# Kernel optimization log

Hardware: AMD Instinct MI355X
Metric: run time of the kernel (lower is better)

## Reference

```python
import jax, jax.numpy as jnp
import numpy as np


def setup_inputs() -> dict:
    key = jax.random.key(0)
    k1, k2 = jax.random.split(key)
    B, S, D, O = 4, 4096, 2048, 2048
    inputs = jax.random.normal(k1, (B, S, D), dtype=jnp.float32)
    # truncated-normal-like init with stddev 1/sqrt(fan_in)
    w = jax.random.normal(k2, (D, O), dtype=jnp.float32) * (1.0 / np.sqrt(D))
    b = jnp.zeros((O,), dtype=jnp.float32)
    return {"inputs": inputs, "w": w, "b": b}


def reference(inputs, w, b):
    # logsumexp-semiring linear layer (basis=None path):
    #   out = log(exp(inputs - max_in) @ exp(w - max_w)) + max_in + max_w + b
    max_inputs = jnp.max(inputs)          # global scalar max for stabilization
    max_w = jnp.max(w)
    exp_inputs = jnp.exp(inputs - max_inputs)   # [B, S, D]
    exp_w = jnp.exp(w - max_w)                  # [D, O]
    out = jnp.log(jnp.dot(exp_inputs, exp_w))   # [B, S, O]
    out = out + (max_inputs + max_w)
    out = out + b                               # broadcast bias over [B, S, O]
    return out
```

## Files before the change

### kernel.cpp

```cpp
#include <hip/hip_runtime.h>

typedef int   i32x4v __attribute__((ext_vector_type(4)));
typedef int   i32x8v __attribute__((ext_vector_type(8)));
typedef float f32x16 __attribute__((ext_vector_type(16)));

#define GLOBAL_AS(p) ((const __attribute__((address_space(1))) void*)(p))
#define LDS_AS(p)    ((__attribute__((address_space(3))) void*)(p))
#define BAR()     __builtin_amdgcn_s_barrier()
#define VMCNT(n)  asm volatile("s_waitcnt vmcnt(" #n ")" ::: "memory")

__device__ inline int fp4_code(float v) {
  return (v > 0.25f) + (v > 0.75f) + (v > 1.25f) + (v > 1.75f) +
         (v > 2.5f) + (v > 3.5f) + (v > 5.0f);
}

__global__ void expcvt_a4_kernel(const float* __restrict__ x,
                                 unsigned char* __restrict__ A4,
                                 unsigned char* __restrict__ SAt,
                                 int M, int K) {
  const int NKB = K >> 5;
  const int t = blockIdx.x * blockDim.x + threadIdx.x;
  const int m = t / NKB, kb = t - m * NKB;
  if (m >= M) return;
  const float4* xs4 = (const float4*)(x + (size_t)m * K + kb * 32);
  float a[32];
  float bm = -3.0e38f;
#pragma unroll
  for (int j = 0; j < 8; ++j) {
    float4 v = xs4[j];
    a[4 * j] = v.x; a[4 * j + 1] = v.y; a[4 * j + 2] = v.z; a[4 * j + 3] = v.w;
    bm = fmaxf(bm, fmaxf(fmaxf(v.x, v.y), fmaxf(v.z, v.w)));
  }
  int e = (int)ceilf(bm * 1.44269504f - 2.58496250f);
  e = min(127, max(-126, e));
  SAt[(size_t)kb * M + ((m >> 7) << 7) + ((m & 31) << 2) + ((m >> 5) & 3)] =
      (unsigned char)(e + 127);
  uint4 u;
  unsigned d[4];
#pragma unroll
  for (int g = 0; g < 4; ++g) {
    unsigned acc = 0;
#pragma unroll
    for (int j = 0; j < 8; ++j) {
      float v = exp2f(a[g * 8 + j] * 1.44269504f - (float)e);
      acc |= (unsigned)fp4_code(v) << (4 * j);
    }
    d[g] = acc;
  }
  u.x = d[0]; u.y = d[1]; u.z = d[2]; u.w = d[3];
  *(uint4*)(A4 + (size_t)m * (K >> 1) + kb * 16) = u;
}

__global__ void expcvt_wt4_kernel(const float* __restrict__ w,
                                  unsigned char* __restrict__ Bt4,
                                  unsigned char* __restrict__ SBt,
                                  int D, int O) {
  __shared__ float tile[32][33];
  int c0 = blockIdx.x * 32;
  int r0 = blockIdx.y * 32;
  int tx = threadIdx.x;
  int ty = threadIdx.y;
#pragma unroll
  for (int j = 0; j < 4; ++j) {
    int r = r0 + ty + j * 8;
    tile[ty + j * 8][tx] = __expf(w[(size_t)r * O + c0 + tx]);
  }
  __syncthreads();
  if (ty == 0) {
    const int n = c0 + tx;
    float bm = 0.0f;
#pragma unroll
    for (int d = 0; d < 32; ++d) bm = fmaxf(bm, tile[d][tx]);
    int e = (int)ceilf(__log2f(bm) - 2.58496250f);
    e = min(127, max(-126, e));
    SBt[(size_t)(r0 >> 5) * O + ((n >> 7) << 7) + ((n & 31) << 2) +
        ((n >> 5) & 3)] = (unsigned char)(e + 127);
    const float inv = exp2f(-(float)e);
    uint4 u;
    unsigned d4[4];
#pragma unroll
    for (int g = 0; g < 4; ++g) {
      unsigned acc = 0;
#pragma unroll
      for (int j = 0; j < 8; ++j)
        acc |= (unsigned)fp4_code(tile[g * 8 + j][tx] * inv) << (4 * j);
      d4[g] = acc;
    }
    u.x = d4[0]; u.y = d4[1]; u.z = d4[2]; u.w = d4[3];
    *(uint4*)(Bt4 + (size_t)n * (D >> 1) + (r0 >> 1)) = u;
  }
}


#define MFMA4(MB, NB, AV, BV, SAv, SBv)                                      \
  acc[MB][NB] = __builtin_amdgcn_mfma_scale_f32_32x32x64_f8f6f4(             \
      AV, BV, acc[MB][NB], 4, 4, 0, SAv, 0, SBv);

#define SCALES(T, S0, S1, S2, S3)                                            \
  {                                                                          \
    const int tt = ((T) < NTK) ? (T) : NTK - 1;                              \
    S0 = *(const int*)(pSA + (size_t)(tt * 4) * M);                          \
    S1 = *(const int*)(pSA + (size_t)(tt * 4 + 2) * M);                      \
    S2 = *(const int*)(pSB + (size_t)(tt * 4) * N);                          \
    S3 = *(const int*)(pSB + (size_t)(tt * 4 + 2) * N);                      \
  }

__global__ __launch_bounds__(256, 4) void gemm_mx4h_kernel(
    const unsigned char* __restrict__ A4, const unsigned char* __restrict__ Bt4,
    const unsigned char* __restrict__ SAt, const unsigned char* __restrict__ SBt,
    const float* __restrict__ bias, float* __restrict__ out,
    int M, int N, int K) {
  __shared__ char lds[32768];

  const int tid = threadIdx.x;
  const int wid = tid >> 6, lane = tid & 63;
  const int wr = wid >> 1, wc = wid & 1;
  const int l31 = lane & 31, lk = lane >> 5;
  const int NTK = K >> 7;
  const size_t Kb = (size_t)K >> 1;

  const int cpx = gridDim.x >> 3;
  const int v   = (blockIdx.x & 7) * cpx + (blockIdx.x >> 3);
  const int nbn = N >> 7;
  const int bm  = v / nbn, bn = v % nbn;
  const int brow = bm << 7, bcol = bn << 7;

  const int swz = ((l31 & 6) << 3) ^ (l31 & 16);
  const int cR0 = (lk << 5) ^ swz;

  const char* gA[2];
  const char* gB[2];
#pragma unroll
  for (int i = 0; i < 2; ++i) {
    const int o = i * 4096 + tid * 16, row = o >> 6;
    const int sg = (((row & 6) << 3) ^ (row & 16)) >> 4;
    const int gl = ((o >> 4) & 3) ^ sg;
    const int gs = ((gl & 1) << 1) | (gl >> 1);
    gA[i] = (const char*)A4 + (size_t)(brow + row) * Kb + (gs << 4);
    gB[i] = (const char*)Bt4 + (size_t)(bcol + row) * Kb + (gs << 4);
  }
  const char* pSA = (const char*)SAt + (size_t)lk * M + brow + l31 * 4;
  const char* pSB = (const char*)SBt + (size_t)lk * N + bcol + l31 * 4;

  auto STAGE = [&](int t, char* base) {
    const int tt = (t < NTK) ? t : NTK - 1;
    const int koff = tt << 6;
#pragma unroll
    for (int i = 0; i < 2; ++i) {
      __builtin_amdgcn_global_load_lds(GLOBAL_AS(gA[i] + koff),
          LDS_AS(base + i * 4096 + wid * 1024), 16, 0, 0);
      __builtin_amdgcn_global_load_lds(GLOBAL_AS(gB[i] + koff),
          LDS_AS(base + 8192 + i * 4096 + wid * 1024), 16, 0, 0);
    }
  };

  f32x16 acc[2][2];
#pragma unroll
  for (int m = 0; m < 2; ++m)
#pragma unroll
    for (int n = 0; n < 2; ++n) acc[m][n] = (f32x16)0.0f;

  const int shA = wr << 4;
  const int shB = wc << 4;

  auto COMPUTE = [&](const char* base, int sa0w, int sa1w, int sb0w, int sb1w) {
    const char* bA = base + wr * 4096;
    const char* bB = base + 8192 + wc * 4096;
#pragma unroll
    for (int h = 0; h < 2; ++h) {
      const int ch = cR0 ^ (h << 4);
      i32x8v a8[2], b8[2];
#pragma unroll
      for (int mb = 0; mb < 2; ++mb) {
        i32x4v f = *(const i32x4v*)(bA + (mb * 32 + l31) * 64 + ch);
        a8[mb] = __builtin_shufflevector(f, f, 0, 1, 2, 3, -1, -1, -1, -1);
      }
#pragma unroll
      for (int nb = 0; nb < 2; ++nb) {
        i32x4v f = *(const i32x4v*)(bB + (nb * 32 + l31) * 64 + ch);
        b8[nb] = __builtin_shufflevector(f, f, 0, 1, 2, 3, -1, -1, -1, -1);
      }
      const int saw = h ? sa1w : sa0w;
      const int sbw = h ? sb1w : sb0w;
      const int sA0 = (saw >> shA) & 0xFF, sA1 = (saw >> (shA + 8)) & 0xFF;
      const int sB0 = (sbw >> shB) & 0xFF, sB1 = (sbw >> (shB + 8)) & 0xFF;
      MFMA4(0, 0, a8[0], b8[0], sA0, sB0)
      MFMA4(1, 0, a8[1], b8[0], sA1, sB0)
      MFMA4(0, 1, a8[0], b8[1], sA0, sB1)
      MFMA4(1, 1, a8[1], b8[1], sA1, sB1)
    }
  };

  char* const L0 = lds;
  char* const L1 = lds + 16384;

  int sE0, sE1, sE2, sE3, sO0, sO1, sO2, sO3;

  STAGE(0, L0);
  SCALES(0, sE0, sE1, sE2, sE3);

  for (int j = 0; j < (NTK >> 1); ++j) {
    STAGE(2 * j + 1, L1);
    SCALES(2 * j + 1, sO0, sO1, sO2, sO3);
    VMCNT(8);
    BAR();
    COMPUTE(L0, sE0, sE1, sE2, sE3);
    BAR();
    STAGE(2 * j + 2, L0);
    SCALES(2 * j + 2, sE0, sE1, sE2, sE3);
    VMCNT(8);
    BAR();
    COMPUTE(L1, sO0, sO1, sO2, sO3);
    BAR();
  }

  VMCNT(0);

  const int col0 = bcol + wc * 64 + l31;
  const int row0 = brow + wr * 64 + lk * 4;
  const float bv0 = bias[col0], bv1 = bias[col0 + 32];
#pragma unroll
  for (int mb = 0; mb < 2; ++mb) {
#pragma unroll
    for (int rg = 0; rg < 16; ++rg) {
      const int row = row0 + mb * 32 + (rg & 3) + 8 * (rg >> 2);
      const size_t ro = (size_t)row * N + col0;
      __builtin_nontemporal_store(__logf(acc[mb][0][rg]) + bv0, &out[ro]);
      __builtin_nontemporal_store(__logf(acc[mb][1][rg]) + bv1, &out[ro + 32]);
    }
  }
}

extern "C" void kernel_launch(void* const* d_in, const int* in_sizes, int n_in,
                              void* d_out, int out_size, void* d_ws, size_t ws_size,
                              hipStream_t stream) {
  const float* inputs = (const float*)d_in[0];
  const float* w      = (const float*)d_in[1];
  const float* bias   = (const float*)d_in[2];
  float* out = (float*)d_out;

  const int O = in_sizes[2];
  const int D = in_sizes[1] / O;
  const size_t MD = (size_t)in_sizes[0];
  const int M = (int)(MD / (size_t)D);

  unsigned char* ws  = (unsigned char*)d_ws;
  unsigned char* A4  = ws;
  unsigned char* Bt4 = ws + MD / 2;
  unsigned char* SAt = Bt4 + (size_t)O * D / 2;
  unsigned char* SBt = SAt + MD / 32;

  const int nthr = (int)((MD / 32 + 255) / 256);
  expcvt_a4_kernel<<<nthr, 256, 0, stream>>>(inputs, A4, SAt, M, D);

  dim3 tg(O / 32, D / 32);
  expcvt_wt4_kernel<<<tg, dim3(32, 8), 0, stream>>>(w, Bt4, SBt, D, O);

  dim3 grid((M / 128) * (O / 128));
  gemm_mx4h_kernel<<<grid, 256, 0, stream>>>(A4, Bt4, SAt, SBt, bias, out,
                                             M, O, D);
}
```

Measured before the change: 90.67 us.

## Pre-tile FP4 operands into MFMA panels and load directly to registers

The conversion kernels now write the FP4 A and B operands in a blocked panel layout that matches the MFMA fragment order. The GEMM drops the LDS staging, barriers and swizzle, and each wave loads its fragments straight from global memory into registers with a two-stage register double buffer. This removes LDS traffic and synchronisation, but gives up data sharing across waves, so each operand is fetched twice per block from L2. Latency hiding now depends on register prefetch, and launch bounds drop to 3 blocks per CU.

```diff
diff --git a/kernel.cpp b/kernel.cpp
--- a/kernel.cpp
+++ b/kernel.cpp
@@ -4,14 +4,13 @@
 typedef int   i32x8v __attribute__((ext_vector_type(8)));
 typedef float f32x16 __attribute__((ext_vector_type(16)));
 
-#define GLOBAL_AS(p) ((const __attribute__((address_space(1))) void*)(p))
-#define LDS_AS(p)    ((__attribute__((address_space(3))) void*)(p))
-#define BAR()     __builtin_amdgcn_s_barrier()
-#define VMCNT(n)  asm volatile("s_waitcnt vmcnt(" #n ")" ::: "memory")
-
 __device__ inline int fp4_code(float v) {
   return (v > 0.25f) + (v > 0.75f) + (v > 1.25f) + (v > 1.75f) +
          (v > 2.5f) + (v > 3.5f) + (v > 5.0f);
+}
+
+__device__ inline size_t panel_addr(int blk, int t, int h, int r, int sub) {
+  return ((((size_t)blk * 16 + t) * 2 + h) << 12) + ((size_t)r << 5) + (sub << 4);
 }
 
 __global__ void expcvt_a4_kernel(const float* __restrict__ x,
@@ -48,7 +47,7 @@
     d[g] = acc;
   }
   u.x = d[0]; u.y = d[1]; u.z = d[2]; u.w = d[3];
-  *(uint4*)(A4 + (size_t)m * (K >> 1) + kb * 16) = u;
+  *(uint4*)(A4 + panel_addr(m >> 7, kb >> 2, (kb >> 1) & 1, m & 127, kb & 1)) = u;
 }
 
 __global__ void expcvt_wt4_kernel(const float* __restrict__ w,
@@ -68,12 +67,13 @@
   __syncthreads();
   if (ty == 0) {
     const int n = c0 + tx;
+    const int kb = r0 >> 5;
     float bm = 0.0f;
 #pragma unroll
     for (int d = 0; d < 32; ++d) bm = fmaxf(bm, tile[d][tx]);
     int e = (int)ceilf(__log2f(bm) - 2.58496250f);
     e = min(127, max(-126, e));
-    SBt[(size_t)(r0 >> 5) * O + ((n >> 7) << 7) + ((n & 31) << 2) +
+    SBt[(size_t)kb * O + ((n >> 7) << 7) + ((n & 31) << 2) +
         ((n >> 5) & 3)] = (unsigned char)(e + 127);
     const float inv = exp2f(-(float)e);
     uint4 u;
@@ -87,37 +87,57 @@
       d4[g] = acc;
     }
     u.x = d4[0]; u.y = d4[1]; u.z = d4[2]; u.w = d4[3];
-    *(uint4*)(Bt4 + (size_t)n * (D >> 1) + (r0 >> 1)) = u;
-  }
-}
-
-
+    *(uint4*)(Bt4 + panel_addr(n >> 7, kb >> 2, (kb >> 1) & 1, n & 127, kb & 1)) = u;
+  }
+}
+
+
+#define PAD8(f) __builtin_shufflevector(f, f, 0, 1, 2, 3, -1, -1, -1, -1)
 #define MFMA4(MB, NB, AV, BV, SAv, SBv)                                      \
   acc[MB][NB] = __builtin_amdgcn_mfma_scale_f32_32x32x64_f8f6f4(             \
       AV, BV, acc[MB][NB], 4, 4, 0, SAv, 0, SBv);
 
-#define SCALES(T, S0, S1, S2, S3)                                            \
+#define LOADT(T, AF, BF, S0, S1, S2, S3)                                     \
   {                                                                          \
     const int tt = ((T) < NTK) ? (T) : NTK - 1;                              \
+    const char* pa = pA + tt * 8192;                                         \
+    const char* pb = pB + tt * 8192;                                         \
+    AF[0][0] = *(const i32x4v*)(pa);                                         \
+    AF[1][0] = *(const i32x4v*)(pa + 1024);                                  \
+    AF[0][1] = *(const i32x4v*)(pa + 4096);                                  \
+    AF[1][1] = *(const i32x4v*)(pa + 5120);                                  \
+    BF[0][0] = *(const i32x4v*)(pb);                                         \
+    BF[1][0] = *(const i32x4v*)(pb + 1024);                                  \
+    BF[0][1] = *(const i32x4v*)(pb + 4096);                                  \
+    BF[1][1] = *(const i32x4v*)(pb + 5120);                                  \
     S0 = *(const int*)(pSA + (size_t)(tt * 4) * M);                          \
     S1 = *(const int*)(pSA + (size_t)(tt * 4 + 2) * M);                      \
     S2 = *(const int*)(pSB + (size_t)(tt * 4) * N);                          \
     S3 = *(const int*)(pSB + (size_t)(tt * 4 + 2) * N);                      \
   }
 
-__global__ __launch_bounds__(256, 4) void gemm_mx4h_kernel(
-    const unsigned char* __restrict__ A4, const unsigned char* __restrict__ Bt4,
+#define COMPUTE(AF, BF, SA0W, SA1W, SB0W, SB1W)                              \
+  _Pragma("unroll") for (int h = 0; h < 2; ++h) {                            \
+    const int saw = h ? (SA1W) : (SA0W);                                     \
+    const int sbw = h ? (SB1W) : (SB0W);                                     \
+    const int sA0 = (saw >> shA) & 0xFF, sA1 = (saw >> (shA + 8)) & 0xFF;    \
+    const int sB0 = (sbw >> shB) & 0xFF, sB1 = (sbw >> (shB + 8)) & 0xFF;    \
+    MFMA4(0, 0, PAD8(AF[0][h]), PAD8(BF[0][h]), sA0, sB0)                    \
+    MFMA4(1, 0, PAD8(AF[1][h]), PAD8(BF[0][h]), sA1, sB0)                    \
+    MFMA4(0, 1, PAD8(AF[0][h]), PAD8(BF[1][h]), sA0, sB1)                    \
+    MFMA4(1, 1, PAD8(AF[1][h]), PAD8(BF[1][h]), sA1, sB1)                    \
+  }
+
+__global__ __launch_bounds__(256, 3) void gemm_mx4s_kernel(
+    const unsigned char* __restrict__ Ap, const unsigned char* __restrict__ Bp,
     const unsigned char* __restrict__ SAt, const unsigned char* __restrict__ SBt,
     const float* __restrict__ bias, float* __restrict__ out,
     int M, int N, int K) {
-  __shared__ char lds[32768];
-
   const int tid = threadIdx.x;
   const int wid = tid >> 6, lane = tid & 63;
   const int wr = wid >> 1, wc = wid & 1;
   const int l31 = lane & 31, lk = lane >> 5;
   const int NTK = K >> 7;
-  const size_t Kb = (size_t)K >> 1;
 
   const int cpx = gridDim.x >> 3;
   const int v   = (blockIdx.x & 7) * cpx + (blockIdx.x >> 3);
@@ -125,35 +145,14 @@
   const int bm  = v / nbn, bn = v % nbn;
   const int brow = bm << 7, bcol = bn << 7;
 
-  const int swz = ((l31 & 6) << 3) ^ (l31 & 16);
-  const int cR0 = (lk << 5) ^ swz;
-
-  const char* gA[2];
-  const char* gB[2];
-#pragma unroll
-  for (int i = 0; i < 2; ++i) {
-    const int o = i * 4096 + tid * 16, row = o >> 6;
-    const int sg = (((row & 6) << 3) ^ (row & 16)) >> 4;
-    const int gl = ((o >> 4) & 3) ^ sg;
-    const int gs = ((gl & 1) << 1) | (gl >> 1);
-    gA[i] = (const char*)A4 + (size_t)(brow + row) * Kb + (gs << 4);
-    gB[i] = (const char*)Bt4 + (size_t)(bcol + row) * Kb + (gs << 4);
-  }
+  const char* pA = (const char*)Ap + ((size_t)bm << 17) +
+                   ((wr * 64 + l31) << 5) + (lk << 4);
+  const char* pB = (const char*)Bp + ((size_t)bn << 17) +
+                   ((wc * 64 + l31) << 5) + (lk << 4);
+
   const char* pSA = (const char*)SAt + (size_t)lk * M + brow + l31 * 4;
   const char* pSB = (const char*)SBt + (size_t)lk * N + bcol + l31 * 4;
 
-  auto STAGE = [&](int t, char* base) {
-    const int tt = (t < NTK) ? t : NTK - 1;
-    const int koff = tt << 6;
-#pragma unroll
-    for (int i = 0; i < 2; ++i) {
-      __builtin_amdgcn_global_load_lds(GLOBAL_AS(gA[i] + koff),
-          LDS_AS(base + i * 4096 + wid * 1024), 16, 0, 0);
-      __builtin_amdgcn_global_load_lds(GLOBAL_AS(gB[i] + koff),
-          LDS_AS(base + 8192 + i * 4096 + wid * 1024), 16, 0, 0);
-    }
-  };
-
   f32x16 acc[2][2];
 #pragma unroll
   for (int m = 0; m < 2; ++m)
@@ -163,58 +162,17 @@
   const int shA = wr << 4;
   const int shB = wc << 4;
 
-  auto COMPUTE = [&](const char* base, int sa0w, int sa1w, int sb0w, int sb1w) {
-    const char* bA = base + wr * 4096;
-    const char* bB = base + 8192 + wc * 4096;
-#pragma unroll
-    for (int h = 0; h < 2; ++h) {
-      const int ch = cR0 ^ (h << 4);
-      i32x8v a8[2], b8[2];
-#pragma unroll
-      for (int mb = 0; mb < 2; ++mb) {
-        i32x4v f = *(const i32x4v*)(bA + (mb * 32 + l31) * 64 + ch);
-        a8[mb] = __builtin_shufflevector(f, f, 0, 1, 2, 3, -1, -1, -1, -1);
-      }
-#pragma unroll
-      for (int nb = 0; nb < 2; ++nb) {
-        i32x4v f = *(const i32x4v*)(bB + (nb * 32 + l31) * 64 + ch);
-        b8[nb] = __builtin_shufflevector(f, f, 0, 1, 2, 3, -1, -1, -1, -1);
-      }
-      const int saw = h ? sa1w : sa0w;
-      const int sbw = h ? sb1w : sb0w;
-      const int sA0 = (saw >> shA) & 0xFF, sA1 = (saw >> (shA + 8)) & 0xFF;
-      const int sB0 = (sbw >> shB) & 0xFF, sB1 = (sbw >> (shB + 8)) & 0xFF;
-      MFMA4(0, 0, a8[0], b8[0], sA0, sB0)
-      MFMA4(1, 0, a8[1], b8[0], sA1, sB0)
-      MFMA4(0, 1, a8[0], b8[1], sA0, sB1)
-      MFMA4(1, 1, a8[1], b8[1], sA1, sB1)
-    }
-  };
-
-  char* const L0 = lds;
-  char* const L1 = lds + 16384;
-
+  i32x4v aE[2][2], bE[2][2], aO[2][2], bO[2][2];
   int sE0, sE1, sE2, sE3, sO0, sO1, sO2, sO3;
 
-  STAGE(0, L0);
-  SCALES(0, sE0, sE1, sE2, sE3);
+  LOADT(0, aE, bE, sE0, sE1, sE2, sE3);
 
   for (int j = 0; j < (NTK >> 1); ++j) {
-    STAGE(2 * j + 1, L1);
-    SCALES(2 * j + 1, sO0, sO1, sO2, sO3);
-    VMCNT(8);
-    BAR();
-    COMPUTE(L0, sE0, sE1, sE2, sE3);
-    BAR();
-    STAGE(2 * j + 2, L0);
-    SCALES(2 * j + 2, sE0, sE1, sE2, sE3);
-    VMCNT(8);
-    BAR();
-    COMPUTE(L1, sO0, sO1, sO2, sO3);
-    BAR();
-  }
-
-  VMCNT(0);
+    LOADT(2 * j + 1, aO, bO, sO0, sO1, sO2, sO3);
+    COMPUTE(aE, bE, sE0, sE1, sE2, sE3);
+    LOADT(2 * j + 2, aE, bE, sE0, sE1, sE2, sE3);
+    COMPUTE(aO, bO, sO0, sO1, sO2, sO3);
+  }
 
   const int col0 = bcol + wc * 64 + l31;
   const int row0 = brow + wr * 64 + lk * 4;
@@ -257,6 +215,6 @@
   expcvt_wt4_kernel<<<tg, dim3(32, 8), 0, stream>>>(w, Bt4, SBt, D, O);
 
   dim3 grid((M / 128) * (O / 128));
-  gemm_mx4h_kernel<<<grid, 256, 0, stream>>>(A4, Bt4, SAt, SBt, bias, out,
+  gemm_mx4s_kernel<<<grid, 256, 0, stream>>>(A4, Bt4, SAt, SBt, bias, out,
                                              M, O, D);
 }
```

New measurement: 90.20 us. About the same (-0.5%).
